# Kernel tuning notes

Hardware: AMD Instinct MI355X
Metric: run time of the kernel (lower is better)

Reference implementation:

```python
import jax, jax.numpy as jnp
import numpy as np

N_NODES = 100000
N_EDGES = 1600000
D_NODE = 96
D_EDGE = 32
N_GRAPHS = 128
BN_EPS = 1e-5


def setup_inputs() -> dict:
    key = jax.random.key(0)
    ks = jax.random.split(key, 8)
    x = jax.random.normal(ks[0], (N_NODES, D_NODE), dtype=jnp.float32)
    edge_attr = jax.random.normal(ks[1], (N_EDGES, D_EDGE), dtype=jnp.float32)
    edge_index = jax.random.randint(ks[2], (2, N_EDGES), 0, N_NODES, dtype=jnp.int64)
    batch = jnp.sort(jax.random.randint(ks[3], (N_NODES,), 0, N_GRAPHS, dtype=jnp.int64))
    W1 = jax.random.normal(ks[4], (16, D_NODE + D_EDGE), dtype=jnp.float32) * 0.09
    b1 = jax.random.normal(ks[5], (16,), dtype=jnp.float32) * 0.01
    gamma = jnp.ones((16,), dtype=jnp.float32)
    beta = jnp.zeros((16,), dtype=jnp.float32)
    run_mean = jnp.zeros((16,), dtype=jnp.float32)
    run_var = jnp.ones((16,), dtype=jnp.float32)
    W2 = jax.random.normal(ks[6], (1, 16), dtype=jnp.float32) * 0.25
    b2 = jax.random.normal(ks[7], (1,), dtype=jnp.float32) * 0.01
    return {"x": x, "edge_attr": edge_attr, "edge_index": edge_index, "batch": batch,
            "W1": W1, "b1": b1, "gamma": gamma, "beta": beta,
            "run_mean": run_mean, "run_var": run_var, "W2": W2, "b2": b2}


def reference(x, edge_attr, edge_index, batch, W1, b1, gamma, beta, run_mean, run_var, W2, b2):
    src, dst = edge_index[0], edge_index[1]
    # per-edge message: MLP(cat([x_j, edge_attr]))  -- [E, d_node+d_edge]
    msg_in = jnp.concatenate([x[src], edge_attr], axis=1)
    h = msg_in @ W1.T + b1                                  # [E, 16]
    # BatchNorm1d in eval mode (running stats); Dropout is identity in eval
    h = gamma * (h - run_mean) * jax.lax.rsqrt(run_var + BN_EPS) + beta
    h = jax.nn.relu(h)
    msg = h @ W2.T + b2                                     # [E, 1]
    # scatter-add messages to target nodes
    node_out = jax.ops.segment_sum(msg, dst, num_segments=N_NODES)   # [N, 1]
    # global add pool per graph
    pooled = jax.ops.segment_sum(node_out, batch, num_segments=N_GRAPHS)  # [G, 1]
    # mean over feature dim (size 1)
    return jnp.mean(pooled, axis=1)                         # [G]
```

## Files before the change

kernel.cpp:

```cpp
#include <hip/hip_runtime.h>
#include <hip/hip_bf16.h>

#define N_NODES 100000
#define N_EDGES 1600000
#define D_NODE 96
#define D_EDGE 32
#define N_GRAPHS 128
#define BN_EPS 1e-5f

#define EDGE_BLOCKS 1024
#define EDGE_THREADS 256

static __device__ __forceinline__ unsigned short f2bf(float f) {
    __hip_bfloat16 h = __float2bfloat16(f);
    return *reinterpret_cast<unsigned short*>(&h);
}
static __device__ __forceinline__ void unpack_bf16x2(unsigned u, float& lo, float& hi) {
    lo = __uint_as_float(u << 16);
    hi = __uint_as_float(u & 0xFFFF0000u);
}

__global__ __launch_bounds__(256) void prep_kernel(
    const float* __restrict__ W1, const float* __restrict__ b1,
    const float* __restrict__ gamma, const float* __restrict__ beta,
    const float* __restrict__ rmean, const float* __restrict__ rvar,
    const float* __restrict__ W2, const float* __restrict__ b2,
    float* __restrict__ w1n, float* __restrict__ w1e, float* __restrict__ cw) {
    int idx = blockIdx.x * 256 + threadIdx.x;
    if (idx < 1536) {
        int k = idx / 96, j = idx % 96;
        float A = gamma[k] * rsqrtf(rvar[k] + BN_EPS);
        w1n[idx] = A * W1[k * (D_NODE + D_EDGE) + j];
    } else if (idx < 2048) {
        int r = idx - 1536;
        int k = r / 32, j = r % 32;
        float A = gamma[k] * rsqrtf(rvar[k] + BN_EPS);
        w1e[r] = A * W1[k * (D_NODE + D_EDGE) + D_NODE + j];
    } else if (idx < 2064) {
        int k = idx - 2048;
        float A = gamma[k] * rsqrtf(rvar[k] + BN_EPS);
        cw[k] = A * (b1[k] - rmean[k]) + beta[k];
    } else if (idx < 2080) {
        int k = idx - 2064;
        cw[16 + k] = W2[k];
    } else if (idx == 2080) {
        cw[32] = b2[0];
    }
}

__global__ __launch_bounds__(256) void node_proj_kernel(const float* __restrict__ x,
                                                        const float* __restrict__ w1n,
                                                        unsigned short* __restrict__ y) {
    __shared__ __align__(16) float sw[16 * 96];
    for (int i = threadIdx.x; i < 16 * 96; i += 256) sw[i] = w1n[i];
    __syncthreads();

    int n = blockIdx.x * 256 + threadIdx.x;
    if (n >= N_NODES) return;

    const float4* xr = (const float4*)(x + (size_t)n * D_NODE);
    float acc[16];
#pragma unroll
    for (int k = 0; k < 16; ++k) acc[k] = 0.f;
#pragma unroll
    for (int j4 = 0; j4 < D_NODE / 4; ++j4) {
        float4 xv = xr[j4];
#pragma unroll
        for (int k = 0; k < 16; ++k) {
            float4 w = *(const float4*)&sw[k * 96 + j4 * 4];
            acc[k] = fmaf(xv.x, w.x, acc[k]);
            acc[k] = fmaf(xv.y, w.y, acc[k]);
            acc[k] = fmaf(xv.z, w.z, acc[k]);
            acc[k] = fmaf(xv.w, w.w, acc[k]);
        }
    }
    unsigned w[8];
#pragma unroll
    for (int i = 0; i < 8; ++i)
        w[i] = (unsigned)f2bf(acc[2 * i]) | ((unsigned)f2bf(acc[2 * i + 1]) << 16);
    uint4* yr = (uint4*)(y + (size_t)n * 16);
    yr[0] = make_uint4(w[0], w[1], w[2], w[3]);
    yr[1] = make_uint4(w[4], w[5], w[6], w[7]);
}

__global__ __launch_bounds__(EDGE_THREADS) void edge_kernel(
    const float* __restrict__ ea, const int* __restrict__ eidx,
    const int* __restrict__ batch, const unsigned short* __restrict__ y,
    const float* __restrict__ w1e, const float* __restrict__ cw,
    float* __restrict__ partials) {
    __shared__ __align__(16) float sw[16 * 32];
    __shared__ float scw[33];
    __shared__ float bins[N_GRAPHS];
    int t = threadIdx.x;
    for (int i = t; i < 16 * 32; i += EDGE_THREADS) sw[i] = w1e[i];
    if (t < 33) scw[t] = cw[t];
    if (t < N_GRAPHS) bins[t] = 0.f;
    __syncthreads();

    const int* srcp = eidx;
    const int* dstp = eidx + N_EDGES;

    for (int e = blockIdx.x * EDGE_THREADS + t; e < N_EDGES; e += EDGE_BLOCKS * EDGE_THREADS) {
        int s = srcp[e];
        int d = dstp[e];

        const float4* er = (const float4*)(ea + (size_t)e * D_EDGE);
        float4 ev[8];
#pragma unroll
        for (int i = 0; i < 8; ++i) ev[i] = er[i];

        const uint4* yrow = (const uint4*)(y + (size_t)s * 16);
        uint4 y0 = yrow[0], y1 = yrow[1];
        float ya[16];
        unpack_bf16x2(y0.x, ya[0], ya[1]);
        unpack_bf16x2(y0.y, ya[2], ya[3]);
        unpack_bf16x2(y0.z, ya[4], ya[5]);
        unpack_bf16x2(y0.w, ya[6], ya[7]);
        unpack_bf16x2(y1.x, ya[8], ya[9]);
        unpack_bf16x2(y1.y, ya[10], ya[11]);
        unpack_bf16x2(y1.z, ya[12], ya[13]);
        unpack_bf16x2(y1.w, ya[14], ya[15]);

        float msg = scw[32];
#pragma unroll
        for (int k = 0; k < 16; ++k) {
            const float4* wr = (const float4*)&sw[k * 32];
            float z = 0.f;
#pragma unroll
            for (int i = 0; i < 8; ++i) {
                float4 w = wr[i];
                z = fmaf(ev[i].x, w.x, z);
                z = fmaf(ev[i].y, w.y, z);
                z = fmaf(ev[i].z, w.z, z);
                z = fmaf(ev[i].w, w.w, z);
            }
            float h = z + ya[k] + scw[k];
            msg = fmaf(fmaxf(h, 0.f), scw[16 + k], msg);
        }

        int g = batch[d];
        atomicAdd(&bins[g], msg);
    }

    __syncthreads();
    if (t < N_GRAPHS) partials[(size_t)blockIdx.x * N_GRAPHS + t] = bins[t];
}

__global__ __launch_bounds__(256) void reduce_kernel(const float* __restrict__ partials,
                                                     float* __restrict__ out) {
    __shared__ float s[256];
    int g = blockIdx.x;
    float acc = 0.f;
    for (int b = threadIdx.x; b < EDGE_BLOCKS; b += 256)
        acc += partials[(size_t)b * N_GRAPHS + g];
    s[threadIdx.x] = acc;
    __syncthreads();
    for (int w = 128; w > 0; w >>= 1) {
        if (threadIdx.x < w) s[threadIdx.x] += s[threadIdx.x + w];
        __syncthreads();
    }
    if (threadIdx.x == 0) out[g] = s[0];
}

extern "C" void kernel_launch(void* const* d_in, const int* in_sizes, int n_in,
                              void* d_out, int out_size, void* d_ws, size_t ws_size,
                              hipStream_t stream) {
    const float* x     = (const float*)d_in[0];
    const float* ea    = (const float*)d_in[1];
    const int*   eidx  = (const int*)d_in[2];
    const int*   batch = (const int*)d_in[3];
    const float* W1    = (const float*)d_in[4];
    const float* b1    = (const float*)d_in[5];
    const float* gamma = (const float*)d_in[6];
    const float* beta  = (const float*)d_in[7];
    const float* rmean = (const float*)d_in[8];
    const float* rvar  = (const float*)d_in[9];
    const float* W2    = (const float*)d_in[10];
    const float* b2    = (const float*)d_in[11];
    float* out = (float*)d_out;

    float* ws = (float*)d_ws;
    float*          w1n      = ws;
    float*          w1e      = ws + 1536;
    float*          cw       = ws + 2048;
    unsigned short* y        = (unsigned short*)(ws + 4096);
    float*          partials = ws + 4096 + 800000;

    prep_kernel<<<9, 256, 0, stream>>>(W1, b1, gamma, beta, rmean, rvar, W2, b2, w1n, w1e, cw);
    node_proj_kernel<<<(N_NODES + 255) / 256, 256, 0, stream>>>(x, w1n, y);
    edge_kernel<<<EDGE_BLOCKS, EDGE_THREADS, 0, stream>>>(ea, eidx, batch, y, w1e, cw, partials);
    reduce_kernel<<<N_GRAPHS, 256, 0, stream>>>(partials, out);
}
```

Baseline: 427.4 us.

## Software-pipeline edge loads, read weights via scalar loads, fold bias into node projection

The edge loop now prefetches the next iteration's edge attributes, source row and graph id before computing the current edge, and streams edge attributes with nontemporal loads. Weights are read directly from global memory as uniform values instead of being staged in LDS, and the bias constant is folded into the node projection. This is meant to hide gather latency and cut LDS traffic in the memory-bound edge pass. In exchange it uses more registers, and launch bounds now request 3 blocks per CU. Folding the bias before the bf16 rounding slightly changes precision.

```diff
diff --git a/kernel.cpp b/kernel.cpp
--- a/kernel.cpp
+++ b/kernel.cpp
@@ -10,6 +10,10 @@
 
 #define EDGE_BLOCKS 1024
 #define EDGE_THREADS 256
+#define EDGE_STRIDE (EDGE_BLOCKS * EDGE_THREADS)
+
+typedef float vfloat4 __attribute__((ext_vector_type(4)));
+typedef unsigned vuint4 __attribute__((ext_vector_type(4)));
 
 static __device__ __forceinline__ unsigned short f2bf(float f) {
     __hip_bfloat16 h = __float2bfloat16(f);
@@ -50,67 +54,87 @@
 
 __global__ __launch_bounds__(256) void node_proj_kernel(const float* __restrict__ x,
                                                         const float* __restrict__ w1n,
+                                                        const float* __restrict__ cw,
                                                         unsigned short* __restrict__ y) {
-    __shared__ __align__(16) float sw[16 * 96];
-    for (int i = threadIdx.x; i < 16 * 96; i += 256) sw[i] = w1n[i];
-    __syncthreads();
-
     int n = blockIdx.x * 256 + threadIdx.x;
     if (n >= N_NODES) return;
 
-    const float4* xr = (const float4*)(x + (size_t)n * D_NODE);
+    const vfloat4* xr = (const vfloat4*)(x + (size_t)n * D_NODE);
     float acc[16];
 #pragma unroll
-    for (int k = 0; k < 16; ++k) acc[k] = 0.f;
+    for (int k = 0; k < 16; ++k) acc[k] = cw[k];
 #pragma unroll
     for (int j4 = 0; j4 < D_NODE / 4; ++j4) {
-        float4 xv = xr[j4];
+        vfloat4 xv = xr[j4];
 #pragma unroll
         for (int k = 0; k < 16; ++k) {
-            float4 w = *(const float4*)&sw[k * 96 + j4 * 4];
-            acc[k] = fmaf(xv.x, w.x, acc[k]);
-            acc[k] = fmaf(xv.y, w.y, acc[k]);
-            acc[k] = fmaf(xv.z, w.z, acc[k]);
-            acc[k] = fmaf(xv.w, w.w, acc[k]);
+            const float* w = w1n + k * D_NODE + j4 * 4;
+            acc[k] = fmaf(xv.x, w[0], acc[k]);
+            acc[k] = fmaf(xv.y, w[1], acc[k]);
+            acc[k] = fmaf(xv.z, w[2], acc[k]);
+            acc[k] = fmaf(xv.w, w[3], acc[k]);
         }
     }
-    unsigned w[8];
+    unsigned p[8];
 #pragma unroll
     for (int i = 0; i < 8; ++i)
-        w[i] = (unsigned)f2bf(acc[2 * i]) | ((unsigned)f2bf(acc[2 * i + 1]) << 16);
-    uint4* yr = (uint4*)(y + (size_t)n * 16);
-    yr[0] = make_uint4(w[0], w[1], w[2], w[3]);
-    yr[1] = make_uint4(w[4], w[5], w[6], w[7]);
-}
-
-__global__ __launch_bounds__(EDGE_THREADS) void edge_kernel(
+        p[i] = (unsigned)f2bf(acc[2 * i]) | ((unsigned)f2bf(acc[2 * i + 1]) << 16);
+    vuint4* yr = (vuint4*)(y + (size_t)n * 16);
+    yr[0] = vuint4{p[0], p[1], p[2], p[3]};
+    yr[1] = vuint4{p[4], p[5], p[6], p[7]};
+}
+
+__global__ __launch_bounds__(EDGE_THREADS, 3) void edge_kernel(
     const float* __restrict__ ea, const int* __restrict__ eidx,
     const int* __restrict__ batch, const unsigned short* __restrict__ y,
     const float* __restrict__ w1e, const float* __restrict__ cw,
     float* __restrict__ partials) {
-    __shared__ __align__(16) float sw[16 * 32];
-    __shared__ float scw[33];
     __shared__ float bins[N_GRAPHS];
     int t = threadIdx.x;
-    for (int i = t; i < 16 * 32; i += EDGE_THREADS) sw[i] = w1e[i];
-    if (t < 33) scw[t] = cw[t];
     if (t < N_GRAPHS) bins[t] = 0.f;
     __syncthreads();
 
     const int* srcp = eidx;
     const int* dstp = eidx + N_EDGES;
 
-    for (int e = blockIdx.x * EDGE_THREADS + t; e < N_EDGES; e += EDGE_BLOCKS * EDGE_THREADS) {
-        int s = srcp[e];
-        int d = dstp[e];
-
-        const float4* er = (const float4*)(ea + (size_t)e * D_EDGE);
-        float4 ev[8];
-#pragma unroll
-        for (int i = 0; i < 8; ++i) ev[i] = er[i];
-
-        const uint4* yrow = (const uint4*)(y + (size_t)s * 16);
-        uint4 y0 = yrow[0], y1 = yrow[1];
+    int e = blockIdx.x * EDGE_THREADS + t;
+
+    vfloat4 nev[8];
+    vuint4 ny0, ny1;
+    int ng = 0;
+    bool valid = e < N_EDGES;
+    if (valid) {
+        int s = srcp[e], d = dstp[e];
+        const vfloat4* er = (const vfloat4*)(ea + (size_t)e * D_EDGE);
+#pragma unroll
+        for (int i = 0; i < 8; ++i) nev[i] = __builtin_nontemporal_load(er + i);
+        const vuint4* yr = (const vuint4*)(y + (size_t)s * 16);
+        ny0 = yr[0];
+        ny1 = yr[1];
+        ng = batch[d];
+    }
+
+    while (valid) {
+        vfloat4 ev[8];
+#pragma unroll
+        for (int i = 0; i < 8; ++i) ev[i] = nev[i];
+        vuint4 y0 = ny0, y1 = ny1;
+        int g = ng;
+
+        int e2 = e + EDGE_STRIDE;
+        valid = e2 < N_EDGES;
+        if (valid) {
+            int s = srcp[e2], d = dstp[e2];
+            const vfloat4* er = (const vfloat4*)(ea + (size_t)e2 * D_EDGE);
+#pragma unroll
+            for (int i = 0; i < 8; ++i) nev[i] = __builtin_nontemporal_load(er + i);
+            const vuint4* yr = (const vuint4*)(y + (size_t)s * 16);
+            ny0 = yr[0];
+            ny1 = yr[1];
+            ng = batch[d];
+        }
+        e = e2;
+
         float ya[16];
         unpack_bf16x2(y0.x, ya[0], ya[1]);
         unpack_bf16x2(y0.y, ya[2], ya[3]);
@@ -121,24 +145,22 @@
         unpack_bf16x2(y1.z, ya[12], ya[13]);
         unpack_bf16x2(y1.w, ya[14], ya[15]);
 
-        float msg = scw[32];
+        float msg = cw[32];
 #pragma unroll
         for (int k = 0; k < 16; ++k) {
-            const float4* wr = (const float4*)&sw[k * 32];
+            const float* wr = w1e + k * D_EDGE;
             float z = 0.f;
 #pragma unroll
             for (int i = 0; i < 8; ++i) {
-                float4 w = wr[i];
-                z = fmaf(ev[i].x, w.x, z);
-                z = fmaf(ev[i].y, w.y, z);
-                z = fmaf(ev[i].z, w.z, z);
-                z = fmaf(ev[i].w, w.w, z);
+                z = fmaf(ev[i].x, wr[i * 4 + 0], z);
+                z = fmaf(ev[i].y, wr[i * 4 + 1], z);
+                z = fmaf(ev[i].z, wr[i * 4 + 2], z);
+                z = fmaf(ev[i].w, wr[i * 4 + 3], z);
             }
-            float h = z + ya[k] + scw[k];
-            msg = fmaf(fmaxf(h, 0.f), scw[16 + k], msg);
+            float h = z + ya[k];
+            msg = fmaf(fmaxf(h, 0.f), cw[16 + k], msg);
         }
 
-        int g = batch[d];
         atomicAdd(&bins[g], msg);
     }
 
@@ -187,7 +209,7 @@
     float*          partials = ws + 4096 + 800000;
 
     prep_kernel<<<9, 256, 0, stream>>>(W1, b1, gamma, beta, rmean, rvar, W2, b2, w1n, w1e, cw);
-    node_proj_kernel<<<(N_NODES + 255) / 256, 256, 0, stream>>>(x, w1n, y);
+    node_proj_kernel<<<(N_NODES + 255) / 256, 256, 0, stream>>>(x, w1n, cw, y);
     edge_kernel<<<EDGE_BLOCKS, EDGE_THREADS, 0, stream>>>(ea, eidx, batch, y, w1e, cw, partials);
     reduce_kernel<<<N_GRAPHS, 256, 0, stream>>>(partials, out);
 }
```

Result: faster. 417.7 us (-2.3%).
